# Optimization experiments

Measured on AMD Instinct MI355X. Metric: run time of the kernel, lower is better.

## Reference

```python
import jax, jax.numpy as jnp
import numpy as np

N = 16384      # total nodes (hits)
K = 8          # n_neighbors
NB = 8         # number of graphs in batch
IN_C = 6       # in_channels
HID = 128      # hidden_channels
NCLS = 3       # num_classes
SLOPE = 0.2    # GATv2 leaky_relu negative_slope
BIG = 1e30     # mask value for cross-graph pairs


def setup_inputs() -> dict:
    key = jax.random.key(0)
    ks = jax.random.split(key, 32)
    coord = jax.random.normal(ks[0], (N, 3), dtype=jnp.float32)
    feat = jax.random.normal(ks[1], (N, IN_C), dtype=jnp.float32)
    batch = jnp.sort(jax.random.randint(ks[2], (N,), 0, NB)).astype(jnp.int32)

    def lin_w(k, fan_in, fan_out):
        return (jax.random.normal(k, (fan_in, fan_out), dtype=jnp.float32)
                * np.float32(1.0 / np.sqrt(fan_in)))

    inp = {"coord": coord, "feat": feat, "batch": batch}
    dims = [IN_C, HID, HID]  # input dim of each of the 3 GATv2 layers
    kidx = 3
    for l, din in enumerate(dims):
        inp[f"Wl{l}"] = lin_w(ks[kidx], din, HID); kidx += 1
        inp[f"bl{l}"] = jnp.zeros((HID,), jnp.float32)
        inp[f"Wr{l}"] = lin_w(ks[kidx], din, HID); kidx += 1
        inp[f"br{l}"] = jnp.zeros((HID,), jnp.float32)
        inp[f"att{l}"] = (jax.random.normal(ks[kidx], (HID,), dtype=jnp.float32)
                          * np.float32(1.0 / np.sqrt(HID))); kidx += 1
        inp[f"bias{l}"] = jnp.zeros((HID,), jnp.float32)
    inp["Wf"] = lin_w(ks[kidx], HID, NCLS)
    inp["bf"] = jnp.zeros((NCLS,), jnp.float32)
    return inp


def knn_idx(coord, batch):
    # pairwise squared distances, masked so neighbors stay within the same graph
    d2 = jnp.sum((coord[:, None, :] - coord[None, :, :]) ** 2, axis=-1)  # [N,N]
    d2 = jnp.where(batch[:, None] == batch[None, :], d2, BIG)
    _, idx = jax.lax.top_k(-d2, K)  # [N,K] nearest (includes self at dist 0)
    return idx


def gatv2_layer(x, idx, Wl, bl, Wr, br, att, bias):
    xl = x @ Wl + bl                         # [N,H] source transform
    xr = x @ Wr + br                         # [N,H] target transform
    g = xl[idx]                              # [N,K,H] gather neighbor features
    e = jax.nn.leaky_relu(g + xr[:, None, :], SLOPE)
    logits = e @ att                         # [N,K] attention scores
    alpha = jax.nn.softmax(logits, axis=1)   # softmax over each node's K nbrs
    return jnp.einsum('nk,nkh->nh', alpha, g) + bias


def reference(coord, feat, batch,
              Wl0, bl0, Wr0, br0, att0, bias0,
              Wl1, bl1, Wr1, br1, att1, bias1,
              Wl2, bl2, Wr2, br2, att2, bias2,
              Wf, bf):
    idx = knn_idx(coord, batch)
    x = jax.nn.relu(gatv2_layer(feat, idx, Wl0, bl0, Wr0, br0, att0, bias0))
    x = jax.nn.relu(gatv2_layer(x, idx, Wl1, bl1, Wr1, br1, att1, bias1))
    x = jax.nn.relu(gatv2_layer(x, idx, Wl2, bl2, Wr2, br2, att2, bias2))
    return x @ Wf + bf
```

## Files before the change

kernel.cpp:

```cpp
#include <hip/hip_runtime.h>
#include <hip/hip_bf16.h>
#include <float.h>
#include <limits.h>

#define NNODES 16384
#define KNB 8
#define HIDC 128
#define KNN_CAP 2528

__device__ __forceinline__ float wave_sum(float x) {
  x += __int_as_float(__builtin_amdgcn_update_dpp(0, __float_as_int(x), 0xB1, 0xF, 0xF, true));
  x += __int_as_float(__builtin_amdgcn_update_dpp(0, __float_as_int(x), 0x4E, 0xF, 0xF, true));
  x += __int_as_float(__builtin_amdgcn_update_dpp(0, __float_as_int(x), 0x124, 0xF, 0xF, true));
  x += __int_as_float(__builtin_amdgcn_update_dpp(0, __float_as_int(x), 0x128, 0xF, 0xF, true));
  float r0 = __int_as_float(__builtin_amdgcn_readlane(__float_as_int(x), 0));
  float r1 = __int_as_float(__builtin_amdgcn_readlane(__float_as_int(x), 16));
  float r2 = __int_as_float(__builtin_amdgcn_readlane(__float_as_int(x), 32));
  float r3 = __int_as_float(__builtin_amdgcn_readlane(__float_as_int(x), 48));
  return (r0 + r1) + (r2 + r3);
}

__device__ __forceinline__ float wave_min_f32(float x) {
  x = fminf(x, __int_as_float(__builtin_amdgcn_update_dpp(0, __float_as_int(x), 0xB1, 0xF, 0xF, true)));
  x = fminf(x, __int_as_float(__builtin_amdgcn_update_dpp(0, __float_as_int(x), 0x4E, 0xF, 0xF, true)));
  x = fminf(x, __int_as_float(__builtin_amdgcn_update_dpp(0, __float_as_int(x), 0x124, 0xF, 0xF, true)));
  x = fminf(x, __int_as_float(__builtin_amdgcn_update_dpp(0, __float_as_int(x), 0x128, 0xF, 0xF, true)));
  float r0 = __int_as_float(__builtin_amdgcn_readlane(__float_as_int(x), 0));
  float r1 = __int_as_float(__builtin_amdgcn_readlane(__float_as_int(x), 16));
  float r2 = __int_as_float(__builtin_amdgcn_readlane(__float_as_int(x), 32));
  float r3 = __int_as_float(__builtin_amdgcn_readlane(__float_as_int(x), 48));
  return fminf(fminf(r0, r1), fminf(r2, r3));
}

__device__ __forceinline__ float dist2(float ax, float ay, float az,
                                       float bx, float by, float bz) {
  float dx = ax - bx, dy = ay - by, dz = az - bz;
  return fmaf(dz, dz, fmaf(dy, dy, dx * dx));
}

#define INS8V(_d, a0, a1, a2, a3, a4, a5, a6, a7)  \
  do {                                             \
    a7 = __builtin_amdgcn_fmed3f(_d, a6, a7);      \
    a6 = __builtin_amdgcn_fmed3f(_d, a5, a6);      \
    a5 = __builtin_amdgcn_fmed3f(_d, a4, a5);      \
    a4 = __builtin_amdgcn_fmed3f(_d, a3, a4);      \
    a3 = __builtin_amdgcn_fmed3f(_d, a2, a3);      \
    a2 = __builtin_amdgcn_fmed3f(_d, a1, a2);      \
    a1 = __builtin_amdgcn_fmed3f(_d, a0, a1);      \
    a0 = fminf(a0, _d);                            \
  } while (0)

__device__ __forceinline__ float merge_T(float l0, float l1, float l2, float l3,
                                         float l4, float l5, float l6, float l7,
                                         int lane) {
  float T = 0.f;
  #pragma unroll
  for (int r = 0; r < KNB; ++r) {
    float m = wave_min_f32(l0);
    T = m;
    unsigned long long msk = __ballot(l0 == m);
    int p = (int)__builtin_ctzll(msk);
    if (lane == p) { l0 = l1; l1 = l2; l2 = l3; l3 = l4; l4 = l5; l5 = l6; l6 = l7; l7 = FLT_MAX; }
  }
  return T;
}

__device__ void knn_global_single(const float* __restrict__ coord,
                                  float qx, float qy, float qz,
                                  int s, int e, int lane,
                                  int* __restrict__ knn_row) {
  float l0 = FLT_MAX, l1 = FLT_MAX, l2 = FLT_MAX, l3 = FLT_MAX,
        l4 = FLT_MAX, l5 = FLT_MAX, l6 = FLT_MAX, l7 = FLT_MAX;
  for (int base = s; base < e; base += 64) {
    int j = base + lane;
    bool ok = j < e;
    int jc = ok ? j : s;
    float d = dist2(coord[jc*3+0], coord[jc*3+1], coord[jc*3+2], qx, qy, qz);
    d = ok ? d : FLT_MAX;
    INS8V(d, l0, l1, l2, l3, l4, l5, l6, l7);
  }
  float T = merge_T(l0, l1, l2, l3, l4, l5, l6, l7, lane);
  unsigned long long lt = (1ull << lane) - 1ull;
  int cnt = 0;
  for (int base = s; base < e; base += 64) {
    int j = base + lane;
    bool ok = j < e;
    int jc = ok ? j : s;
    float d = dist2(coord[jc*3+0], coord[jc*3+1], coord[jc*3+2], qx, qy, qz);
    bool win = ok && (d <= T);
    unsigned long long msk = __ballot(win);
    if (msk) {
      int slot = cnt + __popcll(msk & lt);
      if (win && slot < KNB) knn_row[slot] = j;
      cnt += __popcll(msk);
    }
  }
}

__global__ void seg_kernel(const int* __restrict__ batch, int* __restrict__ seg) {
  int b = threadIdx.x;
  if (b > 8) return;
  int lo = 0, hi = NNODES;
  while (lo < hi) { int m = (lo + hi) >> 1; if (batch[m] < b) lo = m + 1; else hi = m; }
  seg[b] = lo;
}

__global__ __launch_bounds__(512, 8) void knnlin_kernel(
    const float* __restrict__ coord, const int* __restrict__ batch,
    const float* __restrict__ feat,
    const float* __restrict__ Wl0, const float* __restrict__ bl0,
    const float* __restrict__ Wr0, const float* __restrict__ br0,
    const int* __restrict__ seg,
    int* __restrict__ knn, float* __restrict__ xl, float* __restrict__ xr) {
  __shared__ float xs[KNN_CAP];
  __shared__ float ys[KNN_CAP];
  __shared__ float zs[KNN_CAP];
  int t = threadIdx.x;
  int lane = t & 63;
  int wid = t >> 6;
  int n0 = blockIdx.x * 16;

  int b0 = batch[n0];
  int blast = batch[n0 + 15];
  int smin = seg[b0];
  int emax = seg[blast + 1];
  int win_end = min(emax, smin + KNN_CAP);
  int cnt_fill = win_end - smin;

  for (int i = t; i < cnt_fill; i += 512) {
    const float* cp = coord + (size_t)(smin + i) * 3;
    xs[i] = cp[0]; ys[i] = cp[1]; zs[i] = cp[2];
  }
  __syncthreads();

  int nA = n0 + wid * 2, nB = nA + 1;
  int bA = batch[nA], bB = batch[nB];
  int sA = seg[bA], eA = seg[bA + 1];
  bool fast = (bA == bB) && (eA - smin <= KNN_CAP);

  float ax = coord[nA*3+0], ay = coord[nA*3+1], az = coord[nA*3+2];
  float bx = coord[nB*3+0], by = coord[nB*3+1], bz = coord[nB*3+2];

  if (fast) {
    int lo_i = sA - smin;
    int M = eA - sA;
    int F4 = M >> 8;

    float a0 = FLT_MAX, a1 = FLT_MAX, a2 = FLT_MAX, a3 = FLT_MAX,
          a4 = FLT_MAX, a5 = FLT_MAX, a6 = FLT_MAX, a7 = FLT_MAX;
    float b0r = FLT_MAX, b1 = FLT_MAX, b2 = FLT_MAX, b3 = FLT_MAX,
          b4 = FLT_MAX, b5 = FLT_MAX, b6 = FLT_MAX, b7 = FLT_MAX;
    {
      for (int it = 0; it < F4; ++it) {
        int base = lo_i + (it << 8) + lane;
        #pragma unroll
        for (int q = 0; q < 4; ++q) {
          int i = base + (q << 6);
          float cxv = xs[i], cyv = ys[i], czv = zs[i];
          float dA = dist2(cxv, cyv, czv, ax, ay, az);
          float dB = dist2(cxv, cyv, czv, bx, by, bz);
          INS8V(dA, a0, a1, a2, a3, a4, a5, a6, a7);
          INS8V(dB, b0r, b1, b2, b3, b4, b5, b6, b7);
        }
      }
      for (int base = F4 << 8; base < M; base += 64) {
        int lix = base + lane;
        bool ok = lix < M;
        int i = ok ? (lo_i + lix) : lo_i;
        float cxv = xs[i], cyv = ys[i], czv = zs[i];
        float dA = dist2(cxv, cyv, czv, ax, ay, az);
        float dB = dist2(cxv, cyv, czv, bx, by, bz);
        dA = ok ? dA : FLT_MAX;
        dB = ok ? dB : FLT_MAX;
        INS8V(dA, a0, a1, a2, a3, a4, a5, a6, a7);
        INS8V(dB, b0r, b1, b2, b3, b4, b5, b6, b7);
      }
    }

    float TA = merge_T(a0, a1, a2, a3, a4, a5, a6, a7, lane);
    float TB = merge_T(b0r, b1, b2, b3, b4, b5, b6, b7, lane);

    unsigned long long lt = (1ull << lane) - 1ull;
    int cntA = 0, cntB = 0;
    {
      for (int it = 0; it < F4 && (cntA < KNB || cntB < KNB); ++it) {
        int base = lo_i + (it << 8) + lane;
        int g0 = sA + (it << 8) + lane;
        #pragma unroll
        for (int q = 0; q < 4; ++q) {
          int i = base + (q << 6);
          int gidx = g0 + (q << 6);
          float cxv = xs[i], cyv = ys[i], czv = zs[i];
          float dA = dist2(cxv, cyv, czv, ax, ay, az);
          float dB = dist2(cxv, cyv, czv, bx, by, bz);
          unsigned long long mA = __ballot(dA <= TA);
          if (mA) {
            int slot = cntA + __popcll(mA & lt);
            if ((dA <= TA) && slot < KNB) knn[nA*KNB + slot] = gidx;
            cntA += __popcll(mA);
          }
          unsigned long long mB = __ballot(dB <= TB);
          if (mB) {
            int slot = cntB + __popcll(mB & lt);
            if ((dB <= TB) && slot < KNB) knn[nB*KNB + slot] = gidx;
            cntB += __popcll(mB);
          }
        }
      }
      for (int base = F4 << 8; base < M && (cntA < KNB || cntB < KNB); base += 64) {
        int lix = base + lane;
        bool ok = lix < M;
        int i = ok ? (lo_i + lix) : lo_i;
        float cxv = xs[i], cyv = ys[i], czv = zs[i];
        float dA = dist2(cxv, cyv, czv, ax, ay, az);
        float dB = dist2(cxv, cyv, czv, bx, by, bz);
        int gidx = sA + lix;
        bool wA = ok && (dA <= TA);
        bool wB = ok && (dB <= TB);
        unsigned long long mA = __ballot(wA);
        if (mA) {
          int slot = cntA + __popcll(mA & lt);
          if (wA && slot < KNB) knn[nA*KNB + slot] = gidx;
          cntA += __popcll(mA);
        }
        unsigned long long mB = __ballot(wB);
        if (mB) {
          int slot = cntB + __popcll(mB & lt);
          if (wB && slot < KNB) knn[nB*KNB + slot] = gidx;
          cntB += __popcll(mB);
        }
      }
    }
  } else {
    int sB2 = seg[bB], eB2 = seg[bB + 1];
    knn_global_single(coord, ax, ay, az, sA, eA, lane, knn + (size_t)nA * KNB);
    knn_global_single(coord, bx, by, bz, sB2, eB2, lane, knn + (size_t)nB * KNB);
  }

  {
    int cg = t & 63;
    bool isR = cg >= 32;
    const float* W  = isR ? Wr0 : Wl0;
    const float* bi = isR ? br0 : bl0;
    float* dst      = isR ? xr : xl;
    int wc = (cg & 31) * 4;
    float4 w0 = *(const float4*)(W + 0 * HIDC + wc);
    float4 w1 = *(const float4*)(W + 1 * HIDC + wc);
    float4 w2 = *(const float4*)(W + 2 * HIDC + wc);
    float4 w3 = *(const float4*)(W + 3 * HIDC + wc);
    float4 w4 = *(const float4*)(W + 4 * HIDC + wc);
    float4 w5 = *(const float4*)(W + 5 * HIDC + wc);
    float4 bb = *(const float4*)(bi + wc);
    #pragma unroll
    for (int s2 = 0; s2 < 2; ++s2) {
      int node = n0 + wid * 2 + s2;
      const float* fr = feat + (size_t)node * 6;
      float f0 = fr[0], f1 = fr[1], f2 = fr[2], f3 = fr[3], f4 = fr[4], f5 = fr[5];
      float4 acc = make_float4(0.f, 0.f, 0.f, 0.f);
      acc.x = fmaf(f0, w0.x, acc.x); acc.y = fmaf(f0, w0.y, acc.y);
      acc.z = fmaf(f0, w0.z, acc.z); acc.w = fmaf(f0, w0.w, acc.w);
      acc.x = fmaf(f1, w1.x, acc.x); acc.y = fmaf(f1, w1.y, acc.y);
      acc.z = fmaf(f1, w1.z, acc.z); acc.w = fmaf(f1, w1.w, acc.w);
      acc.x = fmaf(f2, w2.x, acc.x); acc.y = fmaf(f2, w2.y, acc.y);
      acc.z = fmaf(f2, w2.z, acc.z); acc.w = fmaf(f2, w2.w, acc.w);
      acc.x = fmaf(f3, w3.x, acc.x); acc.y = fmaf(f3, w3.y, acc.y);
      acc.z = fmaf(f3, w3.z, acc.z); acc.w = fmaf(f3, w3.w, acc.w);
      acc.x = fmaf(f4, w4.x, acc.x); acc.y = fmaf(f4, w4.y, acc.y);
      acc.z = fmaf(f4, w4.z, acc.z); acc.w = fmaf(f4, w4.w, acc.w);
      acc.x = fmaf(f5, w5.x, acc.x); acc.y = fmaf(f5, w5.y, acc.y);
      acc.z = fmaf(f5, w5.z, acc.z); acc.w = fmaf(f5, w5.w, acc.w);
      float4 o;
      o.x = acc.x + bb.x; o.y = acc.y + bb.y;
      o.z = acc.z + bb.z; o.w = acc.w + bb.w;
      *(float4*)(dst + (size_t)node * HIDC + wc) = o;
    }
  }
}

__global__ __launch_bounds__(256) void lin2_kernel(
    const float* __restrict__ x,
    const float* __restrict__ Wl, const float* __restrict__ bl,
    const float* __restrict__ Wr, const float* __restrict__ br,
    float* __restrict__ xl, float* __restrict__ xr) {
  __shared__ float xshm[16 * HIDC];
  int t = threadIdx.x;
  int node0 = blockIdx.x * 16;
  for (int i = t; i < 16 * HIDC; i += 256) xshm[i] = x[node0 * HIDC + i];
  __syncthreads();
  int cg = t & 63;
  int ng = t >> 6;
  int c0 = cg * 4;
  bool isR = (c0 >= HIDC);
  const float* W    = isR ? Wr : Wl;
  const float* bias = isR ? br : bl;
  float* dst        = isR ? xr : xl;
  int wc = isR ? (c0 - HIDC) : c0;

  float4 acc[4];
  #pragma unroll
  for (int nn = 0; nn < 4; ++nn) acc[nn] = make_float4(0.f, 0.f, 0.f, 0.f);

  for (int k0 = 0; k0 < HIDC; k0 += 4) {
    float4 xv[4];
    #pragma unroll
    for (int nn = 0; nn < 4; ++nn)
      xv[nn] = *(const float4*)&xshm[(ng * 4 + nn) * HIDC + k0];
    #pragma unroll
    for (int q = 0; q < 4; ++q) {
      float4 w = *(const float4*)(W + (size_t)(k0 + q) * HIDC + wc);
      #pragma unroll
      for (int nn = 0; nn < 4; ++nn) {
        float xq = (q == 0) ? xv[nn].x : (q == 1) ? xv[nn].y : (q == 2) ? xv[nn].z : xv[nn].w;
        acc[nn].x = fmaf(xq, w.x, acc[nn].x);
        acc[nn].y = fmaf(xq, w.y, acc[nn].y);
        acc[nn].z = fmaf(xq, w.z, acc[nn].z);
        acc[nn].w = fmaf(xq, w.w, acc[nn].w);
      }
    }
  }
  float4 b4 = *(const float4*)(bias + wc);
  #pragma unroll
  for (int nn = 0; nn < 4; ++nn) {
    int node = node0 + ng * 4 + nn;
    float4 o;
    o.x = acc[nn].x + b4.x; o.y = acc[nn].y + b4.y;
    o.z = acc[nn].z + b4.z; o.w = acc[nn].w + b4.w;
    *(float4*)(dst + (size_t)node * HIDC + wc) = o;
  }
}

template<bool FINAL>
__global__ __launch_bounds__(256) void gat_attn_kernel(
    const float* __restrict__ xl, const float* __restrict__ xr,
    const int* __restrict__ knn, const float* __restrict__ att,
    const float* __restrict__ bias, float* __restrict__ xout,
    const float* __restrict__ Wf, const float* __restrict__ bf,
    float* __restrict__ out) {
  int wid = threadIdx.x >> 6;
  int lane = threadIdx.x & 63;
  int n = blockIdx.x * 4 + wid;
  int c0 = 2 * lane, c1 = 2 * lane + 1;
  float2 xr2 = *(const float2*)(xr + (size_t)n * HIDC + c0);
  float2 a2  = *(const float2*)(att + c0);
  int myj = (lane < KNB) ? knn[n * KNB + lane] : 0;
  float g0[8], g1[8], lg[8];
  #pragma unroll
  for (int k = 0; k < 8; ++k) {
    int j = __builtin_amdgcn_readlane(myj, k);
    float2 g = *(const float2*)(xl + (size_t)j * HIDC + c0);
    g0[k] = g.x; g1[k] = g.y;
    float e0 = g.x + xr2.x; e0 = (e0 > 0.f) ? e0 : 0.2f * e0;
    float e1 = g.y + xr2.y; e1 = (e1 > 0.f) ? e1 : 0.2f * e1;
    lg[k] = wave_sum(e0 * a2.x + e1 * a2.y);
  }
  float mx = lg[0];
  #pragma unroll
  for (int k = 1; k < 8; ++k) mx = fmaxf(mx, lg[k]);
  float ssum = 0.f, w[8];
  #pragma unroll
  for (int k = 0; k < 8; ++k) { w[k] = __expf(lg[k] - mx); ssum += w[k]; }
  float inv = 1.f / ssum;
  float o0 = 0.f, o1 = 0.f;
  #pragma unroll
  for (int k = 0; k < 8; ++k) { o0 += w[k] * g0[k]; o1 += w[k] * g1[k]; }
  o0 = fmaxf(fmaf(o0, inv, bias[c0]), 0.f);
  o1 = fmaxf(fmaf(o1, inv, bias[c1]), 0.f);
  if (!FINAL) {
    float2 o; o.x = o0; o.y = o1;
    *(float2*)(xout + (size_t)n * HIDC + c0) = o;
  } else {
    #pragma unroll
    for (int cls = 0; cls < 3; ++cls) {
      float p = wave_sum(o0 * Wf[c0 * 3 + cls] + o1 * Wf[c1 * 3 + cls]);
      if (lane == 0) out[n * 3 + cls] = p + bf[cls];
    }
  }
}

extern "C" void kernel_launch(void* const* d_in, const int* in_sizes, int n_in,
                              void* d_out, int out_size, void* d_ws, size_t ws_size,
                              hipStream_t stream) {
  const float* coord = (const float*)d_in[0];
  const float* feat  = (const float*)d_in[1];
  const int*   batch = (const int*)d_in[2];
  const float* Wl0 = (const float*)d_in[3];
  const float* bl0 = (const float*)d_in[4];
  const float* Wr0 = (const float*)d_in[5];
  const float* br0 = (const float*)d_in[6];
  const float* att0  = (const float*)d_in[7];
  const float* bias0 = (const float*)d_in[8];
  const float* Wl1 = (const float*)d_in[9];
  const float* bl1 = (const float*)d_in[10];
  const float* Wr1 = (const float*)d_in[11];
  const float* br1 = (const float*)d_in[12];
  const float* att1  = (const float*)d_in[13];
  const float* bias1 = (const float*)d_in[14];
  const float* Wl2 = (const float*)d_in[15];
  const float* bl2 = (const float*)d_in[16];
  const float* Wr2 = (const float*)d_in[17];
  const float* br2 = (const float*)d_in[18];
  const float* att2  = (const float*)d_in[19];
  const float* bias2 = (const float*)d_in[20];
  const float* Wf = (const float*)d_in[21];
  const float* bf = (const float*)d_in[22];
  float* out = (float*)d_out;

  char* ws = (char*)d_ws;
  int*   knn = (int*)ws;
  float* xl  = (float*)(ws + (512 << 10));
  float* xr  = xl + (size_t)NNODES * HIDC;
  float* xb0 = xr + (size_t)NNODES * HIDC;
  float* xb1 = xb0 + (size_t)NNODES * HIDC;
  int*   seg = (int*)xb1;

  seg_kernel<<<1, 16, 0, stream>>>(batch, seg);
  knnlin_kernel<<<NNODES / 16, 512, 0, stream>>>(coord, batch, feat,
                                                 Wl0, bl0, Wr0, br0, seg, knn, xl, xr);
  gat_attn_kernel<false><<<NNODES / 4, 256, 0, stream>>>(xl, xr, knn, att0, bias0, xb0,
                                                         nullptr, nullptr, nullptr);

  lin2_kernel<<<NNODES / 16, 256, 0, stream>>>(xb0, Wl1, bl1, Wr1, br1, xl, xr);
  gat_attn_kernel<false><<<NNODES / 4, 256, 0, stream>>>(xl, xr, knn, att1, bias1, xb1,
                                                         nullptr, nullptr, nullptr);

  lin2_kernel<<<NNODES / 16, 256, 0, stream>>>(xb1, Wl2, bl2, Wr2, br2, xl, xr);
  gat_attn_kernel<true><<<NNODES / 4, 256, 0, stream>>>(xl, xr, knn, att2, bias2, nullptr,
                                                        Wf, bf, out);
}
```

Before: 138.2 us.

## Fold segment search into kNN kernel, pack coords, enlarge lin tiles, vector-load indices

Removes the separate seg_kernel launch and has each kNN block binary-search the batch segment boundaries into shared memory. Coordinates in shared memory are packed as float2 xy plus z so each point takes two LDS reads instead of three. lin2 now processes 32 nodes per block with 8 accumulators per thread, which halves the grid and reuses each weight load across more nodes at the cost of more registers. The attention kernel loads neighbor indices as two int4 vectors instead of using readlane broadcasts.

```diff
diff --git a/kernel.cpp b/kernel.cpp
--- a/kernel.cpp
+++ b/kernel.cpp
@@ -97,45 +97,44 @@
   }
 }
 
-__global__ void seg_kernel(const int* __restrict__ batch, int* __restrict__ seg) {
-  int b = threadIdx.x;
-  if (b > 8) return;
-  int lo = 0, hi = NNODES;
-  while (lo < hi) { int m = (lo + hi) >> 1; if (batch[m] < b) lo = m + 1; else hi = m; }
-  seg[b] = lo;
-}
-
 __global__ __launch_bounds__(512, 8) void knnlin_kernel(
     const float* __restrict__ coord, const int* __restrict__ batch,
     const float* __restrict__ feat,
     const float* __restrict__ Wl0, const float* __restrict__ bl0,
     const float* __restrict__ Wr0, const float* __restrict__ br0,
-    const int* __restrict__ seg,
     int* __restrict__ knn, float* __restrict__ xl, float* __restrict__ xr) {
-  __shared__ float xs[KNN_CAP];
-  __shared__ float ys[KNN_CAP];
-  __shared__ float zs[KNN_CAP];
+  __shared__ float2 xy[KNN_CAP];
+  __shared__ float  zs[KNN_CAP];
+  __shared__ int    segs[9];
   int t = threadIdx.x;
   int lane = t & 63;
   int wid = t >> 6;
   int n0 = blockIdx.x * 16;
 
+  if (t < 9) {
+    int lo = 0, hi = NNODES;
+    while (lo < hi) { int m = (lo + hi) >> 1; if (batch[m] < t) lo = m + 1; else hi = m; }
+    segs[t] = lo;
+  }
+  __syncthreads();
+
   int b0 = batch[n0];
   int blast = batch[n0 + 15];
-  int smin = seg[b0];
-  int emax = seg[blast + 1];
+  int smin = segs[b0];
+  int emax = segs[blast + 1];
   int win_end = min(emax, smin + KNN_CAP);
   int cnt_fill = win_end - smin;
 
   for (int i = t; i < cnt_fill; i += 512) {
     const float* cp = coord + (size_t)(smin + i) * 3;
-    xs[i] = cp[0]; ys[i] = cp[1]; zs[i] = cp[2];
+    xy[i] = make_float2(cp[0], cp[1]);
+    zs[i] = cp[2];
   }
   __syncthreads();
 
   int nA = n0 + wid * 2, nB = nA + 1;
   int bA = batch[nA], bB = batch[nB];
-  int sA = seg[bA], eA = seg[bA + 1];
+  int sA = segs[bA], eA = segs[bA + 1];
   bool fast = (bA == bB) && (eA - smin <= KNN_CAP);
 
   float ax = coord[nA*3+0], ay = coord[nA*3+1], az = coord[nA*3+2];
@@ -156,9 +155,10 @@
         #pragma unroll
         for (int q = 0; q < 4; ++q) {
           int i = base + (q << 6);
-          float cxv = xs[i], cyv = ys[i], czv = zs[i];
-          float dA = dist2(cxv, cyv, czv, ax, ay, az);
-          float dB = dist2(cxv, cyv, czv, bx, by, bz);
+          float2 cv = xy[i];
+          float  cz = zs[i];
+          float dA = dist2(cv.x, cv.y, cz, ax, ay, az);
+          float dB = dist2(cv.x, cv.y, cz, bx, by, bz);
           INS8V(dA, a0, a1, a2, a3, a4, a5, a6, a7);
           INS8V(dB, b0r, b1, b2, b3, b4, b5, b6, b7);
         }
@@ -167,9 +167,10 @@
         int lix = base + lane;
         bool ok = lix < M;
         int i = ok ? (lo_i + lix) : lo_i;
-        float cxv = xs[i], cyv = ys[i], czv = zs[i];
-        float dA = dist2(cxv, cyv, czv, ax, ay, az);
-        float dB = dist2(cxv, cyv, czv, bx, by, bz);
+        float2 cv = xy[i];
+        float  cz = zs[i];
+        float dA = dist2(cv.x, cv.y, cz, ax, ay, az);
+        float dB = dist2(cv.x, cv.y, cz, bx, by, bz);
         dA = ok ? dA : FLT_MAX;
         dB = ok ? dB : FLT_MAX;
         INS8V(dA, a0, a1, a2, a3, a4, a5, a6, a7);
@@ -190,9 +191,10 @@
         for (int q = 0; q < 4; ++q) {
           int i = base + (q << 6);
           int gidx = g0 + (q << 6);
-          float cxv = xs[i], cyv = ys[i], czv = zs[i];
-          float dA = dist2(cxv, cyv, czv, ax, ay, az);
-          float dB = dist2(cxv, cyv, czv, bx, by, bz);
+          float2 cv = xy[i];
+          float  cz = zs[i];
+          float dA = dist2(cv.x, cv.y, cz, ax, ay, az);
+          float dB = dist2(cv.x, cv.y, cz, bx, by, bz);
           unsigned long long mA = __ballot(dA <= TA);
           if (mA) {
             int slot = cntA + __popcll(mA & lt);
@@ -211,9 +213,10 @@
         int lix = base + lane;
         bool ok = lix < M;
         int i = ok ? (lo_i + lix) : lo_i;
-        float cxv = xs[i], cyv = ys[i], czv = zs[i];
-        float dA = dist2(cxv, cyv, czv, ax, ay, az);
-        float dB = dist2(cxv, cyv, czv, bx, by, bz);
+        float2 cv = xy[i];
+        float  cz = zs[i];
+        float dA = dist2(cv.x, cv.y, cz, ax, ay, az);
+        float dB = dist2(cv.x, cv.y, cz, bx, by, bz);
         int gidx = sA + lix;
         bool wA = ok && (dA <= TA);
         bool wB = ok && (dB <= TB);
@@ -232,7 +235,7 @@
       }
     }
   } else {
-    int sB2 = seg[bB], eB2 = seg[bB + 1];
+    int sB2 = segs[bB], eB2 = segs[bB + 1];
     knn_global_single(coord, ax, ay, az, sA, eA, lane, knn + (size_t)nA * KNB);
     knn_global_single(coord, bx, by, bz, sB2, eB2, lane, knn + (size_t)nB * KNB);
   }
@@ -282,10 +285,10 @@
     const float* __restrict__ Wl, const float* __restrict__ bl,
     const float* __restrict__ Wr, const float* __restrict__ br,
     float* __restrict__ xl, float* __restrict__ xr) {
-  __shared__ float xshm[16 * HIDC];
+  __shared__ float xs[32 * HIDC];
   int t = threadIdx.x;
-  int node0 = blockIdx.x * 16;
-  for (int i = t; i < 16 * HIDC; i += 256) xshm[i] = x[node0 * HIDC + i];
+  int node0 = blockIdx.x * 32;
+  for (int i = t; i < 32 * HIDC; i += 256) xs[i] = x[node0 * HIDC + i];
   __syncthreads();
   int cg = t & 63;
   int ng = t >> 6;
@@ -296,20 +299,20 @@
   float* dst        = isR ? xr : xl;
   int wc = isR ? (c0 - HIDC) : c0;
 
-  float4 acc[4];
-  #pragma unroll
-  for (int nn = 0; nn < 4; ++nn) acc[nn] = make_float4(0.f, 0.f, 0.f, 0.f);
+  float4 acc[8];
+  #pragma unroll
+  for (int nn = 0; nn < 8; ++nn) acc[nn] = make_float4(0.f, 0.f, 0.f, 0.f);
 
   for (int k0 = 0; k0 < HIDC; k0 += 4) {
-    float4 xv[4];
+    float4 xv[8];
     #pragma unroll
-    for (int nn = 0; nn < 4; ++nn)
-      xv[nn] = *(const float4*)&xshm[(ng * 4 + nn) * HIDC + k0];
+    for (int nn = 0; nn < 8; ++nn)
+      xv[nn] = *(const float4*)&xs[(ng * 8 + nn) * HIDC + k0];
     #pragma unroll
     for (int q = 0; q < 4; ++q) {
       float4 w = *(const float4*)(W + (size_t)(k0 + q) * HIDC + wc);
       #pragma unroll
-      for (int nn = 0; nn < 4; ++nn) {
+      for (int nn = 0; nn < 8; ++nn) {
         float xq = (q == 0) ? xv[nn].x : (q == 1) ? xv[nn].y : (q == 2) ? xv[nn].z : xv[nn].w;
         acc[nn].x = fmaf(xq, w.x, acc[nn].x);
         acc[nn].y = fmaf(xq, w.y, acc[nn].y);
@@ -320,8 +323,8 @@
   }
   float4 b4 = *(const float4*)(bias + wc);
   #pragma unroll
-  for (int nn = 0; nn < 4; ++nn) {
-    int node = node0 + ng * 4 + nn;
+  for (int nn = 0; nn < 8; ++nn) {
+    int node = node0 + ng * 8 + nn;
     float4 o;
     o.x = acc[nn].x + b4.x; o.y = acc[nn].y + b4.y;
     o.z = acc[nn].z + b4.z; o.w = acc[nn].w + b4.w;
@@ -342,11 +345,13 @@
   int c0 = 2 * lane, c1 = 2 * lane + 1;
   float2 xr2 = *(const float2*)(xr + (size_t)n * HIDC + c0);
   float2 a2  = *(const float2*)(att + c0);
-  int myj = (lane < KNB) ? knn[n * KNB + lane] : 0;
+  int4 ja = *(const int4*)(knn + (size_t)n * KNB);
+  int4 jb = *(const int4*)(knn + (size_t)n * KNB + 4);
   float g0[8], g1[8], lg[8];
   #pragma unroll
   for (int k = 0; k < 8; ++k) {
-    int j = __builtin_amdgcn_readlane(myj, k);
+    int j = (k==0)?ja.x:(k==1)?ja.y:(k==2)?ja.z:(k==3)?ja.w
+          :(k==4)?jb.x:(k==5)?jb.y:(k==6)?jb.z:jb.w;
     float2 g = *(const float2*)(xl + (size_t)j * HIDC + c0);
     g0[k] = g.x; g1[k] = g.y;
     float e0 = g.x + xr2.x; e0 = (e0 > 0.f) ? e0 : 0.2f * e0;
@@ -411,19 +416,17 @@
   float* xr  = xl + (size_t)NNODES * HIDC;
   float* xb0 = xr + (size_t)NNODES * HIDC;
   float* xb1 = xb0 + (size_t)NNODES * HIDC;
-  int*   seg = (int*)xb1;
-
-  seg_kernel<<<1, 16, 0, stream>>>(batch, seg);
+
   knnlin_kernel<<<NNODES / 16, 512, 0, stream>>>(coord, batch, feat,
-                                                 Wl0, bl0, Wr0, br0, seg, knn, xl, xr);
+                                                 Wl0, bl0, Wr0, br0, knn, xl, xr);
   gat_attn_kernel<false><<<NNODES / 4, 256, 0, stream>>>(xl, xr, knn, att0, bias0, xb0,
                                                          nullptr, nullptr, nullptr);
 
-  lin2_kernel<<<NNODES / 16, 256, 0, stream>>>(xb0, Wl1, bl1, Wr1, br1, xl, xr);
+  lin2_kernel<<<NNODES / 32, 256, 0, stream>>>(xb0, Wl1, bl1, Wr1, br1, xl, xr);
   gat_attn_kernel<false><<<NNODES / 4, 256, 0, stream>>>(xl, xr, knn, att1, bias1, xb1,
                                                          nullptr, nullptr, nullptr);
 
-  lin2_kernel<<<NNODES / 16, 256, 0, stream>>>(xb1, Wl2, bl2, Wr2, br2, xl, xr);
+  lin2_kernel<<<NNODES / 32, 256, 0, stream>>>(xb1, Wl2, bl2, Wr2, br2, xl, xr);
   gat_attn_kernel<true><<<NNODES / 4, 256, 0, stream>>>(xl, xr, knn, att2, bias2, nullptr,
                                                         Wf, bf, out);
 }
```

Result: slower. 145.2 us (+5.1%).
